# Kernel optimization log

Hardware: AMD Instinct MI355X
Metric: run time of the kernel (lower is better)

## Reference

```python
import jax, jax.numpy as jnp
import numpy as np

N = 50000
D = 128
E = 600000
R = 8


def setup_inputs() -> dict:
    key = jax.random.key(0)
    ks = jax.random.split(key, 8)
    x = jax.random.normal(ks[0], (N, D), dtype=jnp.float32)
    edge_index = jax.random.randint(ks[1], (2, E), 0, N, dtype=jnp.int64)
    edge_type = jax.random.randint(ks[2], (E,), 0, R, dtype=jnp.int64)
    scale = 1.0 / np.sqrt(D)
    w1 = jax.random.normal(ks[3], (R, D, D), dtype=jnp.float32) * scale
    root1 = jax.random.normal(ks[4], (D, D), dtype=jnp.float32) * scale
    b1 = jnp.zeros((D,), dtype=jnp.float32)
    w2 = jax.random.normal(ks[5], (R, D, D), dtype=jnp.float32) * scale
    root2 = jax.random.normal(ks[6], (D, D), dtype=jnp.float32) * scale
    b2 = jnp.zeros((D,), dtype=jnp.float32)
    return {"x": x, "edge_index": edge_index, "edge_type": edge_type,
            "w1": w1, "root1": root1, "b1": b1,
            "w2": w2, "root2": root2, "b2": b2}


def _rgcn_conv(x, edge_index, edge_type, w, root, b):
    # PyG RGCNConv: per-relation MEAN aggregation of source features over
    # incoming edges, then relation-specific linear, summed over relations,
    # plus root transform and bias.
    src, dst = edge_index[0], edge_index[1]
    # combined segment id: (dst_node, relation) -> one segment_sum pass
    seg = dst * R + edge_type  # [E]
    msgs = x[src]              # [E, D] gather
    sums = jax.ops.segment_sum(msgs, seg, num_segments=N * R).reshape(N, R, D)
    cnts = jax.ops.segment_sum(jnp.ones((msgs.shape[0],), dtype=x.dtype), seg,
                               num_segments=N * R).reshape(N, R, 1)
    mean = sums / jnp.maximum(cnts, 1.0)  # [N, R, D]; empty -> 0
    out = jnp.einsum('nrd,rde->ne', mean, w) + x @ root + b
    return out


def reference(x, edge_index, edge_type, w1, root1, b1, w2, root2, b2):
    # dropout is identity in eval mode
    h = jax.nn.relu(_rgcn_conv(x, edge_index, edge_type, w1, root1, b1))
    out = jax.nn.relu(_rgcn_conv(h, edge_index, edge_type, w2, root2, b2))
    return out
```

## Files before the change

### kernel.cpp

```cpp
#include <hip/hip_runtime.h>

#define NN 50000
#define D 128
#define EE 600000
#define R 8
#define NR (NN * R)
#define SCAN_CHUNK 1024
#define NSB ((NR + SCAN_CHUNK - 1) / SCAN_CHUNK)
#define KO 1152

typedef unsigned short u16;
typedef unsigned int u32;
typedef __attribute__((ext_vector_type(8))) short bf16x8;
typedef __attribute__((ext_vector_type(16))) float f32x16;

__device__ inline u16 f2bf(float f) {
    union { float f; u32 u; } v; v.f = f;
    return (u16)((v.u + 0x7FFFu + ((v.u >> 16) & 1u)) >> 16);
}
__device__ inline float bf2f(u16 h) {
    union { u32 u; float f; } v; v.u = ((u32)h) << 16;
    return v.f;
}

__global__ __launch_bounds__(256) void hist_kernel(const int* __restrict__ dst,
                                                   const int* __restrict__ et,
                                                   int* __restrict__ cnt, int E) {
    int e = blockIdx.x * 256 + threadIdx.x;
    if (e < E) atomicAdd(&cnt[dst[e] * R + et[e]], 1);
}

__global__ __launch_bounds__(256) void scanA(const int* __restrict__ cnt,
                                             int* __restrict__ off,
                                             int* __restrict__ bsum) {
    __shared__ int ts[256];
    const int b = blockIdx.x, t = threadIdx.x;
    const int base = b * SCAN_CHUNK + t * 4;
    int v0 = 0, v1 = 0, v2 = 0, v3 = 0;
    if (base + 3 < NR) {
        int4 q = *(const int4*)(cnt + base);
        v0 = q.x; v1 = q.y; v2 = q.z; v3 = q.w;
    } else {
        if (base < NR) v0 = cnt[base];
        if (base + 1 < NR) v1 = cnt[base + 1];
        if (base + 2 < NR) v2 = cnt[base + 2];
    }
    const int s = v0 + v1 + v2 + v3;
    ts[t] = s;
    __syncthreads();
    for (int d = 1; d < 256; d <<= 1) {
        int x = (t >= d) ? ts[t - d] : 0;
        __syncthreads();
        ts[t] += x;
        __syncthreads();
    }
    const int excl = ts[t] - s;
    if (base < NR) off[base] = excl;
    if (base + 1 < NR) off[base + 1] = excl + v0;
    if (base + 2 < NR) off[base + 2] = excl + v0 + v1;
    if (base + 3 < NR) off[base + 3] = excl + v0 + v1 + v2;
    if (t == 255) bsum[b] = ts[255];
}

__global__ __launch_bounds__(256) void scanBC(int* __restrict__ off,
                                              int* __restrict__ cursor,
                                              const int* __restrict__ bsum) {
    __shared__ int red[256];
    const int b = blockIdx.x, t = threadIdx.x;
    int p = 0;
    for (int i = t; i < b; i += 256) p += bsum[i];
    red[t] = p;
    __syncthreads();
    for (int d = 128; d > 0; d >>= 1) {
        if (t < d) red[t] += red[t + d];
        __syncthreads();
    }
    const int add = red[0];
    const int base = b * SCAN_CHUNK + t * 4;
#pragma unroll
    for (int j = 0; j < 4; ++j)
        if (base + j < NR) {
            int v = off[base + j] + add;
            off[base + j] = v;
            cursor[base + j] = v;
        }
    if (b == 0 && t == 0) off[NR] = EE;
}

__global__ __launch_bounds__(256) void place_kernel(const int* __restrict__ src,
                                                    const int* __restrict__ dst,
                                                    const int* __restrict__ et,
                                                    int* __restrict__ cursor,
                                                    u32* __restrict__ epk, int E) {
    int e = blockIdx.x * 256 + threadIdx.x;
    if (e < E) {
        int r = et[e];
        int key = dst[e] * R + r;
        int p = atomicAdd(&cursor[key], 1);
        epk[p] = ((u32)src[e] << 3) | (u32)r;
    }
}

__global__ __launch_bounds__(256) void bprep2_kernel(const float* __restrict__ w1,
                                                     const float* __restrict__ root1,
                                                     u16* __restrict__ Bf1,
                                                     const float* __restrict__ w2,
                                                     const float* __restrict__ root2,
                                                     u16* __restrict__ Bf2,
                                                     int4* __restrict__ cntz) {
    int gidx = blockIdx.x * 256 + threadIdx.x;
    for (int i = gidx; i < NR / 4; i += 36864)
        cntz[i] = make_int4(0, 0, 0, 0);
    if (gidx >= 2 * 9 * 8 * 4 * 64) return;
    const int layer = gidx / (9 * 8 * 4 * 64);
    const int idx = gidx - layer * (9 * 8 * 4 * 64);
    const float* w = layer ? w2 : w1;
    const float* root = layer ? root2 : root1;
    u16* Bfrag = layer ? Bf2 : Bf1;
    const int lane = idx & 63;
    const int cg = (idx >> 6) & 3;
    const int ks = (idx >> 8) & 7;
    const int ct = idx >> 11;
    const int col = ct * 128 + cg * 32 + (lane & 31);
    const int kbase = ks * 16 + (lane >> 5) * 8;
    u16* o = Bfrag + (size_t)idx * 8;
#pragma unroll
    for (int j = 0; j < 8; ++j) {
        const int k = kbase + j;
        float v = (col < R * D) ? w[(size_t)(col >> 7) * (D * D) + (size_t)k * D + (col & 127)]
                                : root[(size_t)k * D + (col - R * D)];
        o[j] = f2bf(v);
    }
}

template <bool INF32>
__global__ __launch_bounds__(256, 3) void gemm_xw(const void* __restrict__ xin,
                                                  const u16* __restrict__ Bfrag,
                                                  u16* __restrict__ y) {
    __shared__ uint4 Bs[2048];

    const int t = threadIdx.x;
    const int wave = t >> 6;
    const int lane = t & 63;
    const int l31 = lane & 31;
    const int lh = lane >> 5;
    const int rh = wave >> 1;
    const int ch = wave & 1;
    const int n0 = blockIdx.x * 64;
    const int m = n0 + rh * 32 + l31;
    const int mc = (m < NN) ? m : (NN - 1);

    bf16x8 af[8];
    if (INF32) {
        const float* xr = (const float*)xin + (size_t)mc * D + lh * 8;
#pragma unroll
        for (int ks = 0; ks < 8; ++ks) {
            float4 v0 = *(const float4*)(xr + ks * 16);
            float4 v1 = *(const float4*)(xr + ks * 16 + 4);
            bf16x8 a;
            a[0] = (short)f2bf(v0.x); a[1] = (short)f2bf(v0.y);
            a[2] = (short)f2bf(v0.z); a[3] = (short)f2bf(v0.w);
            a[4] = (short)f2bf(v1.x); a[5] = (short)f2bf(v1.y);
            a[6] = (short)f2bf(v1.z); a[7] = (short)f2bf(v1.w);
            af[ks] = a;
        }
    } else {
        const u16* xr = (const u16*)xin + (size_t)mc * D + lh * 8;
#pragma unroll
        for (int ks = 0; ks < 8; ++ks)
            af[ks] = *(const bf16x8*)(xr + ks * 16);
    }

#pragma unroll 1
    for (int ct = 0; ct < 9; ++ct) {
        const uint4* bsrc = (const uint4*)Bfrag + (size_t)ct * 2048 + t;

        __syncthreads();
#pragma unroll
        for (int i = 0; i < 8; ++i) Bs[t + 256 * i] = bsrc[256 * i];
        __syncthreads();

        f32x16 acc0 = (f32x16)(0.f), acc1 = (f32x16)(0.f);
        const u16* bb = (const u16*)Bs + (size_t)(ch * 2) * 512 + lane * 8;
#pragma unroll
        for (int ks = 0; ks < 8; ++ks) {
            bf16x8 b0 = *(const bf16x8*)(bb + (size_t)ks * 2048);
            acc0 = __builtin_amdgcn_mfma_f32_32x32x16_bf16(af[ks], b0, acc0, 0, 0, 0);
            bf16x8 b1 = *(const bf16x8*)(bb + (size_t)ks * 2048 + 512);
            acc1 = __builtin_amdgcn_mfma_f32_32x32x16_bf16(af[ks], b1, acc1, 0, 0, 0);
        }

        const int colb = ct * 128 + ch * 64 + l31;
#pragma unroll
        for (int reg = 0; reg < 16; ++reg) {
            const int rl = (reg & 3) + 8 * (reg >> 2) + 4 * lh;
            const int grow = n0 + rh * 32 + rl;
            if (grow < NN) {
                u16* yp = y + (size_t)grow * KO + colb;
                yp[0] = f2bf(acc0[reg]);
                yp[32] = f2bf(acc1[reg]);
            }
        }
    }
}

template <bool OUTBF>
__global__ __launch_bounds__(256) void agg_kernel(const u32* __restrict__ yv,
                                                  const int* __restrict__ off,
                                                  const u32* __restrict__ epk,
                                                  const int* __restrict__ cnt,
                                                  const float* __restrict__ bias,
                                                  void* __restrict__ outp) {
    const int n = blockIdx.x * 4 + (threadIdx.x >> 6);
    const int lane = threadIdx.x & 63;
    const int e0 = off[n * 8], e1 = off[n * 8 + 8];

    float ax = 0.f, ay = 0.f;
    int cbase = e0;
    u32 yoff = 0u; float sc = 0.f;
    if (cbase + lane < e1) {
        const u32 pk = epk[cbase + lane];
        const int r = (int)(pk & 7u);
        yoff = (pk >> 3) * (KO / 2) + (u32)r * (D / 2);
        sc = 1.0f / (float)cnt[n * 8 + r];
    }

    int i = e0;
    while (i < e1) {
        const int chunk_end = (e1 < cbase + 64) ? e1 : (cbase + 64);
        for (; i + 3 < chunk_end; i += 4) {
            const int j = i - cbase;
            const u32 p0 = (u32)__shfl((int)yoff, j);
            const u32 p1 = (u32)__shfl((int)yoff, j + 1);
            const u32 p2 = (u32)__shfl((int)yoff, j + 2);
            const u32 p3 = (u32)__shfl((int)yoff, j + 3);
            const float f0 = __shfl(sc, j);
            const float f1 = __shfl(sc, j + 1);
            const float f2 = __shfl(sc, j + 2);
            const float f3 = __shfl(sc, j + 3);
            const u32 v0 = yv[(size_t)p0 + lane];
            const u32 v1 = yv[(size_t)p1 + lane];
            const u32 v2 = yv[(size_t)p2 + lane];
            const u32 v3 = yv[(size_t)p3 + lane];
            ax += f0 * bf2f((u16)(v0 & 0xFFFFu)); ay += f0 * bf2f((u16)(v0 >> 16));
            ax += f1 * bf2f((u16)(v1 & 0xFFFFu)); ay += f1 * bf2f((u16)(v1 >> 16));
            ax += f2 * bf2f((u16)(v2 & 0xFFFFu)); ay += f2 * bf2f((u16)(v2 >> 16));
            ax += f3 * bf2f((u16)(v3 & 0xFFFFu)); ay += f3 * bf2f((u16)(v3 >> 16));
        }
        for (; i < chunk_end; ++i) {
            const int j = i - cbase;
            const u32 p0 = (u32)__shfl((int)yoff, j);
            const float f0 = __shfl(sc, j);
            const u32 v0 = yv[(size_t)p0 + lane];
            ax += f0 * bf2f((u16)(v0 & 0xFFFFu));
            ay += f0 * bf2f((u16)(v0 >> 16));
        }
        if (i < e1) {
            cbase += 64;
            if (cbase + lane < e1) {
                const u32 pk = epk[cbase + lane];
                const int r = (int)(pk & 7u);
                yoff = (pk >> 3) * (KO / 2) + (u32)r * (D / 2);
                sc = 1.0f / (float)cnt[n * 8 + r];
            } else { yoff = 0u; sc = 0.f; }
        }
    }

    const u32 rv = yv[(size_t)n * (KO / 2) + (R * D / 2) + lane];
    const float2 bb = ((const float2*)bias)[lane];
    const float ox = fmaxf(ax + bf2f((u16)(rv & 0xFFFFu)) + bb.x, 0.f);
    const float oy = fmaxf(ay + bf2f((u16)(rv >> 16)) + bb.y, 0.f);
    if (OUTBF)
        ((u32*)outp)[(size_t)n * 64 + lane] = (u32)f2bf(ox) | ((u32)f2bf(oy) << 16);
    else
        ((float2*)outp)[(size_t)n * 64 + lane] = make_float2(ox, oy);
}

extern "C" void kernel_launch(void* const* d_in, const int* in_sizes, int n_in,
                              void* d_out, int out_size, void* d_ws, size_t ws_size,
                              hipStream_t stream) {
    const float* x = (const float*)d_in[0];
    const int* ei = (const int*)d_in[1];
    const int* et = (const int*)d_in[2];
    const float* w1 = (const float*)d_in[3];
    const float* root1 = (const float*)d_in[4];
    const float* b1 = (const float*)d_in[5];
    const float* w2 = (const float*)d_in[6];
    const float* root2 = (const float*)d_in[7];
    const float* b2 = (const float*)d_in[8];
    float* out = (float*)d_out;

    char* ws = (char*)d_ws;
    int* off    = (int*)(ws + 0);
    int* cnt_i  = (int*)(ws + 1600512);
    int* cursor = (int*)(ws + 3200512);
    int* bsum   = (int*)(ws + 4800512);
    u32* epk    = (u32*)(ws + 4804096);
    u32* h      = (u32*)(ws + 7204096);
    u16* y      = (u16*)(ws + 20004096);
    u16* Bf1    = (u16*)(ws + 135204096);
    u16* Bf2    = (u16*)(ws + 135499008);

    const int* srcp = ei;
    const int* dstp = ei + EE;

    bprep2_kernel<<<144, 256, 0, stream>>>(w1, root1, Bf1, w2, root2, Bf2,
                                           (int4*)cnt_i);
    hist_kernel<<<(EE + 255) / 256, 256, 0, stream>>>(dstp, et, cnt_i, EE);
    scanA<<<NSB, 256, 0, stream>>>(cnt_i, off, bsum);
    scanBC<<<NSB, 256, 0, stream>>>(off, cursor, bsum);
    place_kernel<<<(EE + 255) / 256, 256, 0, stream>>>(srcp, dstp, et, cursor,
                                                       epk, EE);

    const int gemm_blocks = (NN + 63) / 64;
    const int agg_blocks = NN / 4;

    gemm_xw<true><<<gemm_blocks, 256, 0, stream>>>(x, Bf1, y);
    agg_kernel<true><<<agg_blocks, 256, 0, stream>>>((const u32*)y, off, epk,
                                                     cnt_i, b1, h);

    gemm_xw<false><<<gemm_blocks, 256, 0, stream>>>(h, Bf2, y);
    agg_kernel<false><<<agg_blocks, 256, 0, stream>>>((const u32*)y, off, epk,
                                                      cnt_i, b2, out);
}
```

Baseline: 289.4 us.

## Read GEMM B fragments directly from global memory, dropping LDS staging

The X·W GEMM no longer stages B fragments in shared memory behind two barriers per column tile. Each block now covers 32 rows instead of 64, and each wave computes one 32-column slice, loading its B fragments straight from global memory (L2-resident). This removes the LDS traffic and synchronisation and raises the occupancy hint. In exchange, B reuse across waves drops, giving twice as many blocks and more global/L2 loads of the weight fragments.

```diff
diff --git a/kernel.cpp b/kernel.cpp
--- a/kernel.cpp
+++ b/kernel.cpp
@@ -134,20 +134,16 @@
 }
 
 template <bool INF32>
-__global__ __launch_bounds__(256, 3) void gemm_xw(const void* __restrict__ xin,
+__global__ __launch_bounds__(256, 4) void gemm_xw(const void* __restrict__ xin,
                                                   const u16* __restrict__ Bfrag,
                                                   u16* __restrict__ y) {
-    __shared__ uint4 Bs[2048];
-
     const int t = threadIdx.x;
     const int wave = t >> 6;
     const int lane = t & 63;
     const int l31 = lane & 31;
     const int lh = lane >> 5;
-    const int rh = wave >> 1;
-    const int ch = wave & 1;
-    const int n0 = blockIdx.x * 64;
-    const int m = n0 + rh * 32 + l31;
+    const int n0 = blockIdx.x * 32;
+    const int m = n0 + l31;
     const int mc = (m < NN) ? m : (NN - 1);
 
     bf16x8 af[8];
@@ -173,33 +169,21 @@
 
 #pragma unroll 1
     for (int ct = 0; ct < 9; ++ct) {
-        const uint4* bsrc = (const uint4*)Bfrag + (size_t)ct * 2048 + t;
-
-        __syncthreads();
-#pragma unroll
-        for (int i = 0; i < 8; ++i) Bs[t + 256 * i] = bsrc[256 * i];
-        __syncthreads();
-
-        f32x16 acc0 = (f32x16)(0.f), acc1 = (f32x16)(0.f);
-        const u16* bb = (const u16*)Bs + (size_t)(ch * 2) * 512 + lane * 8;
+        const u16* bp = Bfrag + ((size_t)ct * 32 + wave) * 512 + lane * 8;
+        f32x16 acc = (f32x16)(0.f);
 #pragma unroll
         for (int ks = 0; ks < 8; ++ks) {
-            bf16x8 b0 = *(const bf16x8*)(bb + (size_t)ks * 2048);
-            acc0 = __builtin_amdgcn_mfma_f32_32x32x16_bf16(af[ks], b0, acc0, 0, 0, 0);
-            bf16x8 b1 = *(const bf16x8*)(bb + (size_t)ks * 2048 + 512);
-            acc1 = __builtin_amdgcn_mfma_f32_32x32x16_bf16(af[ks], b1, acc1, 0, 0, 0);
-        }
-
-        const int colb = ct * 128 + ch * 64 + l31;
+            bf16x8 b = *(const bf16x8*)(bp + (size_t)ks * 2048);
+            acc = __builtin_amdgcn_mfma_f32_32x32x16_bf16(af[ks], b, acc, 0, 0, 0);
+        }
+
+        const int colb = ct * 128 + wave * 32 + l31;
 #pragma unroll
         for (int reg = 0; reg < 16; ++reg) {
             const int rl = (reg & 3) + 8 * (reg >> 2) + 4 * lh;
-            const int grow = n0 + rh * 32 + rl;
-            if (grow < NN) {
-                u16* yp = y + (size_t)grow * KO + colb;
-                yp[0] = f2bf(acc0[reg]);
-                yp[32] = f2bf(acc1[reg]);
-            }
+            const int grow = n0 + rl;
+            if (grow < NN)
+                y[(size_t)grow * KO + colb] = f2bf(acc[reg]);
         }
     }
 }
@@ -312,7 +296,7 @@
     place_kernel<<<(EE + 255) / 256, 256, 0, stream>>>(srcp, dstp, et, cursor,
                                                        epk, EE);
 
-    const int gemm_blocks = (NN + 63) / 64;
+    const int gemm_blocks = (NN + 31) / 32;
     const int agg_blocks = NN / 4;
 
     gemm_xw<true><<<gemm_blocks, 256, 0, stream>>>(x, Bf1, y);
```

New measurement: 300.6 us. 1.04x slower.
